# Performance work log

Measured on AMD Instinct MI355X. Metric: run time of the kernel, lower is better.

Reference implementation:

```python
import jax, jax.numpy as jnp
import numpy as np

GRID_LENGTH = 8.0
GRID_SIZE = 32
ATOM_TYPE = 6


def generate_grid(grid_length, grid_size):
    # matches torch generate_grid: x varies slowest, z fastest -> meshgrid 'ij'
    half = grid_length / 2.0
    ticks = jnp.linspace(-half, half, grid_size, dtype=jnp.float32)
    gx, gy, gz = jnp.meshgrid(ticks, ticks, ticks, indexing='ij')
    return jnp.stack([gx, gy, gz], axis=-1)  # (G,G,G,3)


def setup_inputs() -> dict:
    key = jax.random.key(0)
    k1, k2 = jax.random.split(key)
    distance_vector = jax.random.normal(k1, (4, 32, 16, 3), dtype=jnp.float32) * 2.0
    atomic_numbers = jax.random.randint(k2, (32, 16), 0, 10, dtype=jnp.int64 if jax.config.read('jax_enable_x64') else jnp.int32)
    sigma = jnp.ones((1,), dtype=jnp.float32)
    return {"distance_vector": distance_vector, "atomic_numbers": atomic_numbers, "sigma": sigma}


def reference(distance_vector, atomic_numbers, sigma):
    # distance_vector: (B, A, N, 3); atomic_numbers: (A, N); sigma: (1,)
    grid = generate_grid(GRID_LENGTH, GRID_SIZE)  # (G,G,G,3)
    # diff: (B, A, N, G, G, G, 3)
    diff = grid[None, None, None] - distance_vector[:, :, :, None, None, None, :]
    sq = jnp.sum(diff * diff, axis=-1)  # ||grid - dv||^2, (B,A,N,G,G,G)
    coeff = -0.5 / (sigma[0] * sigma[0])
    box = jnp.exp(coeff * sq)
    mask = (atomic_numbers == ATOM_TYPE).astype(box.dtype)  # (A,N)
    # masked sum over neighbor axis N -> (B, A, G, G, G)
    out = jnp.sum(box * mask[None, :, :, None, None, None], axis=2)
    return out
```

## Files before the change

kernel.cpp:

```cpp
#include <hip/hip_runtime.h>
#include <hip/hip_bf16.h>

#define G 32
#define NNBR 16
#define ATOM_TYPE 6

__global__ __launch_bounds__(256) void voxel_kernel(
    const float* __restrict__ dv,
    const int*   __restrict__ an,
    const float* __restrict__ sigma,
    float*       __restrict__ out)
{
    const int ba    = blockIdx.x;
    const int a     = ba & 31;
    const int islab = blockIdx.y;
    const int tid   = threadIdx.x;

    __shared__ __align__(16) float sEx[NNBR][G];
    __shared__ __align__(16) float sEy[NNBR][G];
    __shared__ __align__(16) float sEz[NNBR][G];
    __shared__ float sDv[NNBR * 3];
    __shared__ int   sIdx[NNBR];
    __shared__ int   sM;

    if (tid < NNBR * 3) sDv[tid] = dv[(size_t)ba * (NNBR * 3) + tid];

    int flag = 0;
    if (tid < NNBR) flag = (an[a * NNBR + tid] == ATOM_TYPE) ? 1 : 0;
    unsigned long long mask = __ballot(flag);
    if (flag) {
        int pos = __popcll(mask & ((1ull << tid) - 1ull));
        sIdx[pos] = tid;
    }
    if (tid == 0) sM = (int)__popcll(mask);
    __syncthreads();

    const int   M     = sM;
    const float s     = sigma[0];
    const float coeff = -0.5f / (s * s);
    const float step  = 8.0f / 31.0f;

    for (int idx = tid; idx < M * G; idx += 256) {
        const int m = idx >> 5;
        const int i = idx & 31;
        const int n = sIdx[m];
        const float t  = -4.0f + (float)i * step;
        const float dx = t - sDv[3 * n + 0];
        const float dy = t - sDv[3 * n + 1];
        const float dz = t - sDv[3 * n + 2];
        sEx[m][i] = __expf(coeff * dx * dx);
        sEy[m][i] = __expf(coeff * dy * dy);
        sEz[m][i] = __expf(coeff * dz * dz);
    }
    __syncthreads();

    const int j  = tid >> 3;
    const int k0 = (tid & 7) * 4;
    const int i0 = islab * 4;

    float4 acc0 = {0.f, 0.f, 0.f, 0.f};
    float4 acc1 = acc0, acc2 = acc0, acc3 = acc0;

    for (int m = 0; m < M; ++m) {
        const float  ey = sEy[m][j];
        const float4 ez = *(const float4*)&sEz[m][k0];
        const float4 ex = *(const float4*)&sEx[m][i0];
        const float p0 = ex.x * ey, p1 = ex.y * ey, p2 = ex.z * ey, p3 = ex.w * ey;
        acc0.x += p0 * ez.x; acc0.y += p0 * ez.y; acc0.z += p0 * ez.z; acc0.w += p0 * ez.w;
        acc1.x += p1 * ez.x; acc1.y += p1 * ez.y; acc1.z += p1 * ez.z; acc1.w += p1 * ez.w;
        acc2.x += p2 * ez.x; acc2.y += p2 * ez.y; acc2.z += p2 * ez.z; acc2.w += p2 * ez.w;
        acc3.x += p3 * ez.x; acc3.y += p3 * ez.y; acc3.z += p3 * ez.z; acc3.w += p3 * ez.w;
    }

    float4* out4 = (float4*)(out + (size_t)ba * (G * G * G) + (size_t)islab * 4096);
    out4[0 * 256 + tid] = acc0;
    out4[1 * 256 + tid] = acc1;
    out4[2 * 256 + tid] = acc2;
    out4[3 * 256 + tid] = acc3;
}

extern "C" void kernel_launch(void* const* d_in, const int* in_sizes, int n_in,
                              void* d_out, int out_size, void* d_ws, size_t ws_size,
                              hipStream_t stream) {
    const float* dv    = (const float*)d_in[0];
    const int*   an    = (const int*)d_in[1];
    const float* sigma = (const float*)d_in[2];
    float*       out   = (float*)d_out;

    dim3 grid(4 * 32, 8);
    dim3 block(256);
    voxel_kernel<<<grid, block, 0, stream>>>(dv, an, sigma, out);
}
```

Before: 63.39 us.

## Give each block one x-plane and fold the x factor into the y exponentials

The grid grows from 8 to 32 blocks per (b,a), so each block now computes a single x-plane. Each thread therefore produces one float4 instead of four. The block's x-Gaussian is folded into the y table by computing exp(coeff*(dx^2+dy^2)), which removes the per-iteration products with ex and the sEx shared array. This cuts register use and raises parallelism to fill more CUs, at the cost of four times as many blocks, each redoing the mask ballot and exp table setup.

```diff
diff --git a/kernel.cpp b/kernel.cpp
--- a/kernel.cpp
+++ b/kernel.cpp
@@ -1,5 +1,4 @@
 #include <hip/hip_runtime.h>
-#include <hip/hip_bf16.h>
 
 #define G 32
 #define NNBR 16
@@ -11,14 +10,13 @@
     const float* __restrict__ sigma,
     float*       __restrict__ out)
 {
-    const int ba    = blockIdx.x;
-    const int a     = ba & 31;
-    const int islab = blockIdx.y;
-    const int tid   = threadIdx.x;
+    const int ba  = blockIdx.x;
+    const int a   = ba & 31;
+    const int ip  = blockIdx.y;
+    const int tid = threadIdx.x;
 
-    __shared__ __align__(16) float sEx[NNBR][G];
-    __shared__ __align__(16) float sEy[NNBR][G];
-    __shared__ __align__(16) float sEz[NNBR][G];
+    __shared__ __align__(16) float sEyx[NNBR][G];
+    __shared__ __align__(16) float sEz [NNBR][G];
     __shared__ float sDv[NNBR * 3];
     __shared__ int   sIdx[NNBR];
     __shared__ int   sM;
@@ -39,44 +37,36 @@
     const float s     = sigma[0];
     const float coeff = -0.5f / (s * s);
     const float step  = 8.0f / 31.0f;
+    const float ti    = -4.0f + (float)ip * step;
 
     for (int idx = tid; idx < M * G; idx += 256) {
         const int m = idx >> 5;
-        const int i = idx & 31;
+        const int j = idx & 31;
         const int n = sIdx[m];
-        const float t  = -4.0f + (float)i * step;
-        const float dx = t - sDv[3 * n + 0];
-        const float dy = t - sDv[3 * n + 1];
-        const float dz = t - sDv[3 * n + 2];
-        sEx[m][i] = __expf(coeff * dx * dx);
-        sEy[m][i] = __expf(coeff * dy * dy);
-        sEz[m][i] = __expf(coeff * dz * dz);
+        const float t  = -4.0f + (float)j * step;
+        const float dx = ti - sDv[3 * n + 0];
+        const float dy = t  - sDv[3 * n + 1];
+        const float dz = t  - sDv[3 * n + 2];
+        sEyx[m][j] = __expf(coeff * (dx * dx + dy * dy));
+        sEz [m][j] = __expf(coeff * (dz * dz));
     }
     __syncthreads();
 
     const int j  = tid >> 3;
     const int k0 = (tid & 7) * 4;
-    const int i0 = islab * 4;
 
-    float4 acc0 = {0.f, 0.f, 0.f, 0.f};
-    float4 acc1 = acc0, acc2 = acc0, acc3 = acc0;
-
+    float4 acc = {0.f, 0.f, 0.f, 0.f};
     for (int m = 0; m < M; ++m) {
-        const float  ey = sEy[m][j];
+        const float  e  = sEyx[m][j];
         const float4 ez = *(const float4*)&sEz[m][k0];
-        const float4 ex = *(const float4*)&sEx[m][i0];
-        const float p0 = ex.x * ey, p1 = ex.y * ey, p2 = ex.z * ey, p3 = ex.w * ey;
-        acc0.x += p0 * ez.x; acc0.y += p0 * ez.y; acc0.z += p0 * ez.z; acc0.w += p0 * ez.w;
-        acc1.x += p1 * ez.x; acc1.y += p1 * ez.y; acc1.z += p1 * ez.z; acc1.w += p1 * ez.w;
-        acc2.x += p2 * ez.x; acc2.y += p2 * ez.y; acc2.z += p2 * ez.z; acc2.w += p2 * ez.w;
-        acc3.x += p3 * ez.x; acc3.y += p3 * ez.y; acc3.z += p3 * ez.z; acc3.w += p3 * ez.w;
+        acc.x += e * ez.x;
+        acc.y += e * ez.y;
+        acc.z += e * ez.z;
+        acc.w += e * ez.w;
     }
 
-    float4* out4 = (float4*)(out + (size_t)ba * (G * G * G) + (size_t)islab * 4096);
-    out4[0 * 256 + tid] = acc0;
-    out4[1 * 256 + tid] = acc1;
-    out4[2 * 256 + tid] = acc2;
-    out4[3 * 256 + tid] = acc3;
+    float4* out4 = (float4*)(out + (size_t)ba * (G * G * G) + (size_t)ip * (G * G));
+    out4[tid] = acc;
 }
 
 extern "C" void kernel_launch(void* const* d_in, const int* in_sizes, int n_in,
@@ -87,7 +77,7 @@
     const float* sigma = (const float*)d_in[2];
     float*       out   = (float*)d_out;
 
-    dim3 grid(4 * 32, 8);
+    dim3 grid(4 * 32, G);
     dim3 block(256);
     voxel_kernel<<<grid, block, 0, stream>>>(dv, an, sigma, out);
 }
```

After: 63.86 us. About the same (+0.8%).
